# Performance work log

Hardware: AMD Instinct MI355X
Metric: run time of the kernel (lower is better)

The kernel has to match this reference:

```python
import jax, jax.numpy as jnp
import numpy as np


def setup_inputs() -> dict:
    key = jax.random.key(0)
    k0, k1, k2, k3, k4, k5 = jax.random.split(key, 6)
    B, V, Fin, K, Fout = 8, 49152, 64, 3, 64
    nnz = V * 8  # ~8 neighbors per vertex (HEALPix sphere graph)
    std = (2.0 / (Fin * K)) ** 0.5  # Kaiming-normal as in reset_parameters
    inputs = jax.random.normal(k0, (B, V, Fin), jnp.float32)
    weight = jax.random.normal(k1, (Fin, K, Fout), jnp.float32) * std
    bias = jax.random.normal(k2, (Fout,), jnp.float32) * 0.05
    lap_rows = jax.random.randint(k3, (nnz,), 0, V, jnp.int32)
    lap_cols = jax.random.randint(k4, (nnz,), 0, V, jnp.int32)
    lap_vals = jax.random.normal(k5, (nnz,), jnp.float32) * 0.1
    return {"inputs": inputs, "weight": weight, "bias": bias,
            "lap_rows": lap_rows, "lap_cols": lap_cols, "lap_vals": lap_vals}


def reference(inputs, weight, bias, lap_rows, lap_cols, lap_vals):
    B, V, Fin = inputs.shape
    _, K, Fout = weight.shape

    def spmm(x):  # sparse Laplacian (COO) @ dense [V, Fin*B]
        return jax.ops.segment_sum(lap_vals[:, None] * x[lap_cols], lap_rows,
                                   num_segments=V)

    # x0: [V, Fin*B], matching torch's permute(1,2,0).view(V, Fin*B)
    x0 = inputs.transpose(1, 2, 0).reshape(V, Fin * B)
    xs = [x0]
    if K > 1:
        x1 = spmm(x0)
        xs.append(x1)
    for _ in range(2, K):
        x2 = 2.0 * spmm(x1) - x0  # Chebyshev recurrence
        xs.append(x2)
        x0, x1 = x1, x2
    x = jnp.stack(xs)                                    # [K, V, Fin*B]
    x = x.reshape(K, V, Fin, B).transpose(3, 1, 2, 0)    # [B, V, Fin, K]
    x = x.reshape(B * V, Fin * K)
    out = x @ weight.reshape(Fin * K, Fout)              # dense GEMM
    return out.reshape(B, V, Fout) + bias
```

## Files before the change

### kernel.cpp

```cpp
#include <hip/hip_runtime.h>
#include <stdint.h>

#define B_   8
#define V_   49152
#define M_   (B_ * V_)

typedef unsigned short ushort_t;
typedef __attribute__((ext_vector_type(8))) short short8;
typedef __attribute__((ext_vector_type(4))) float float4v;

__device__ __forceinline__ float bf2f_lo(unsigned int pk) {
    union { unsigned int u; float f; } x; x.u = pk << 16; return x.f;
}
__device__ __forceinline__ float bf2f_hi(unsigned int pk) {
    union { unsigned int u; float f; } x; x.u = pk & 0xffff0000u; return x.f;
}
__device__ __forceinline__ ushort_t f2bf(float f) {
    union { unsigned int u; float f; } x; x.f = f;
    unsigned int u = x.u;
    unsigned int r = u + 0x7fffu + ((u >> 16) & 1u);
    return (ushort_t)(r >> 16);
}
__device__ __forceinline__ unsigned int pack2(float a, float b) {
    return ((unsigned int)f2bf(b) << 16) | (unsigned int)f2bf(a);
}
__device__ __forceinline__ void fma8(float* acc, float w, const uint4& p) {
    const unsigned int* u = (const unsigned int*)&p;
    #pragma unroll
    for (int i = 0; i < 4; i++) {
        acc[2 * i]     += w * bf2f_lo(u[i]);
        acc[2 * i + 1] += w * bf2f_hi(u[i]);
    }
}

__global__ void fill_sentinel(float* out, int n) {
    int i = blockIdx.x * blockDim.x + threadIdx.x;
    if (i < n) out[i] = 9999.0f;
}

__global__ void zero_kernel(int* p, int n) {
    int i = blockIdx.x * blockDim.x + threadIdx.x;
    if (i < n) p[i] = 0;
}

__global__ void hist_kernel(const int* __restrict__ rows, int nnz, int* __restrict__ counts) {
    int i = blockIdx.x * blockDim.x + threadIdx.x;
    if (i < nnz) atomicAdd(&counts[rows[i]], 1);
}

__global__ __launch_bounds__(1024) void scan_kernel(const int* __restrict__ counts,
                                                    int* __restrict__ offsets) {
    __shared__ int s[1024];
    int t = threadIdx.x;
    const int C = V_ / 1024;
    int base_i = t * C;
    int sum = 0;
    for (int j = 0; j < C; j++) sum += counts[base_i + j];
    s[t] = sum;
    __syncthreads();
    for (int off = 1; off < 1024; off <<= 1) {
        int v = (t >= off) ? s[t - off] : 0;
        __syncthreads();
        s[t] += v;
        __syncthreads();
    }
    int run = (t == 0) ? 0 : s[t - 1];
    for (int j = 0; j < C; j++) {
        offsets[base_i + j] = run;
        run += counts[base_i + j];
    }
    if (t == 1023) offsets[V_] = run;
}

__global__ void bucket_kernel(const int* __restrict__ rows, const int* __restrict__ cols,
                              const float* __restrict__ vals, int nnz,
                              const int* __restrict__ offsets, int* __restrict__ cursor,
                              int* __restrict__ e_col, float* __restrict__ e_val) {
    int i = blockIdx.x * blockDim.x + threadIdx.x;
    if (i >= nnz) return;
    int r = rows[i];
    int p = offsets[r] + atomicAdd(&cursor[r], 1);
    e_col[p] = cols[i];
    e_val[p] = vals[i];
}

__global__ __launch_bounds__(256) void prep_x0t(const float* __restrict__ inp,
                                                ushort_t* __restrict__ x0t) {
    int idx = blockIdx.x * 256 + threadIdx.x;
    int f2 = idx & 31, v = idx >> 5;
    #pragma unroll
    for (int b = 0; b < 8; b++) {
        const float* src = inp + ((size_t)b * V_ + v) * 64 + f2 * 2;
        float2 d = *(const float2*)src;
        *(unsigned int*)(x0t + ((size_t)v * 8 + b) * 64 + f2 * 2) = pack2(d.x, d.y);
    }
}

__global__ void prep_w(const float* __restrict__ wgt, ushort_t* __restrict__ wBf) {
    int idx = blockIdx.x * 256 + threadIdx.x;
    if (idx >= 6 * 4 * 64 * 8) return;
    int j = idx & 7, lane = (idx >> 3) & 63, nt = (idx >> 9) & 3, kb = idx >> 11;
    int k = kb * 32 + (lane >> 4) * 8 + j;
    int kc = k >> 6, fi = k & 63;
    int fo = nt * 16 + (lane & 15);
    wBf[idx] = f2bf(wgt[(fi * 3 + kc) * 64 + fo]);
}

__device__ __forceinline__ void gather16(const ushort_t* __restrict__ src,
                                         const int* __restrict__ e_col,
                                         const float* __restrict__ e_val,
                                         int beg, int end, int b, int f8, float* acc) {
    int e = beg;
    for (; e + 4 <= end; e += 4) {
        int c0 = e_col[e], c1 = e_col[e + 1], c2 = e_col[e + 2], c3 = e_col[e + 3];
        float w0 = e_val[e], w1 = e_val[e + 1], w2 = e_val[e + 2], w3 = e_val[e + 3];
        const ushort_t* p0 = src + ((size_t)c0 * 512) + b * 64 + f8 * 16;
        const ushort_t* p1 = src + ((size_t)c1 * 512) + b * 64 + f8 * 16;
        const ushort_t* p2 = src + ((size_t)c2 * 512) + b * 64 + f8 * 16;
        const ushort_t* p3 = src + ((size_t)c3 * 512) + b * 64 + f8 * 16;
        uint4 a0 = *(const uint4*)p0, b0 = *(const uint4*)(p0 + 8);
        uint4 a1 = *(const uint4*)p1, b1 = *(const uint4*)(p1 + 8);
        uint4 a2 = *(const uint4*)p2, b2 = *(const uint4*)(p2 + 8);
        uint4 a3 = *(const uint4*)p3, b3 = *(const uint4*)(p3 + 8);
        fma8(acc, w0, a0); fma8(acc + 8, w0, b0);
        fma8(acc, w1, a1); fma8(acc + 8, w1, b1);
        fma8(acc, w2, a2); fma8(acc + 8, w2, b2);
        fma8(acc, w3, a3); fma8(acc + 8, w3, b3);
    }
    for (; e < end; e++) {
        int c = e_col[e];
        float w = e_val[e];
        const ushort_t* p = src + ((size_t)c * 512) + b * 64 + f8 * 16;
        uint4 a = *(const uint4*)p, bq = *(const uint4*)(p + 8);
        fma8(acc, w, a); fma8(acc + 8, w, bq);
    }
}

__global__ __launch_bounds__(256) void spmm1_kernel(const ushort_t* __restrict__ x0t,
                                                    const int* __restrict__ offsets,
                                                    const int* __restrict__ e_col,
                                                    const float* __restrict__ e_val,
                                                    ushort_t* __restrict__ x1) {
    int t = threadIdx.x;
    int vi = t >> 5, b = (t >> 2) & 7, f8 = t & 3;
    int v = blockIdx.x * 8 + vi;
    float acc[16];
    #pragma unroll
    for (int i = 0; i < 16; i++) acc[i] = 0.f;
    gather16(x0t, e_col, e_val, offsets[v], offsets[v + 1], b, f8, acc);
    unsigned int opk[8];
    #pragma unroll
    for (int i = 0; i < 8; i++) opk[i] = pack2(acc[2 * i], acc[2 * i + 1]);
    ushort_t* dst = x1 + ((size_t)v * 8 + b) * 64 + f8 * 16;
    *(uint4*)dst       = make_uint4(opk[0], opk[1], opk[2], opk[3]);
    *(uint4*)(dst + 8) = make_uint4(opk[4], opk[5], opk[6], opk[7]);
}

__global__ __launch_bounds__(256) void spmm2_gemm(const ushort_t* __restrict__ x0t,
                                                  const ushort_t* __restrict__ x1,
                                                  const int* __restrict__ offsets,
                                                  const int* __restrict__ e_col,
                                                  const float* __restrict__ e_val,
                                                  const ushort_t* __restrict__ wBf,
                                                  const float* __restrict__ bias,
                                                  float* __restrict__ out) {
    __shared__ ushort_t sh[64 * 72];
    int t = threadIdx.x;
    int vi = t >> 5, b = (t >> 2) & 7, f8 = t & 3;
    int v0 = blockIdx.x * 8;
    int v = v0 + vi;
    float acc[16];
    #pragma unroll
    for (int i = 0; i < 16; i++) acc[i] = 0.f;
    gather16(x1, e_col, e_val, offsets[v], offsets[v + 1], b, f8, acc);

    size_t r = (size_t)v * 8 + b;
    const ushort_t* x0p = x0t + r * 64 + f8 * 16;
    uint4 qa = *(const uint4*)x0p, qb = *(const uint4*)(x0p + 8);
    const unsigned int* ua = (const unsigned int*)&qa;
    const unsigned int* ub = (const unsigned int*)&qb;
    unsigned int opk[8];
    #pragma unroll
    for (int i = 0; i < 4; i++)
        opk[i] = pack2(2.f * acc[2 * i] - bf2f_lo(ua[i]),
                       2.f * acc[2 * i + 1] - bf2f_hi(ua[i]));
    #pragma unroll
    for (int i = 0; i < 4; i++)
        opk[4 + i] = pack2(2.f * acc[8 + 2 * i] - bf2f_lo(ub[i]),
                           2.f * acc[8 + 2 * i + 1] - bf2f_hi(ub[i]));
    int mg = vi * 8 + b;
    ushort_t* dst = sh + mg * 72 + f8 * 16;
    *(uint4*)dst       = make_uint4(opk[0], opk[1], opk[2], opk[3]);
    *(uint4*)(dst + 8) = make_uint4(opk[4], opk[5], opk[6], opk[7]);
    __syncthreads();

    int lane = t & 63, wv = t >> 6;
    int quad = lane >> 4, col = lane & 15;

    short8 Bf[6][4];
    #pragma unroll
    for (int kb = 0; kb < 6; kb++)
        #pragma unroll
        for (int nt = 0; nt < 4; nt++)
            Bf[kb][nt] = *(const short8*)(wBf + ((size_t)((kb * 4 + nt) * 64 + lane)) * 8);

    float bv[4];
    #pragma unroll
    for (int nt = 0; nt < 4; nt++) bv[nt] = bias[nt * 16 + col];

    float4v accm[4];
    #pragma unroll
    for (int nt = 0; nt < 4; nt++) accm[nt] = (float4v){0.f, 0.f, 0.f, 0.f};

    int m0 = v0 * 8 + wv * 16;
    size_t arow = (size_t)(m0 + col) * 64 + quad * 8;
    #pragma unroll
    for (int p = 0; p < 2; p++) {
        short8 A = *(const short8*)(x0t + arow + p * 32);
        #pragma unroll
        for (int nt = 0; nt < 4; nt++)
            accm[nt] = __builtin_amdgcn_mfma_f32_16x16x32_bf16(A, Bf[p][nt], accm[nt], 0, 0, 0);
    }
    #pragma unroll
    for (int p = 0; p < 2; p++) {
        short8 A = *(const short8*)(x1 + arow + p * 32);
        #pragma unroll
        for (int nt = 0; nt < 4; nt++)
            accm[nt] = __builtin_amdgcn_mfma_f32_16x16x32_bf16(A, Bf[2 + p][nt], accm[nt], 0, 0, 0);
    }
    #pragma unroll
    for (int p = 0; p < 2; p++) {
        short8 A = *(const short8*)(sh + (wv * 16 + col) * 72 + quad * 8 + p * 32);
        #pragma unroll
        for (int nt = 0; nt < 4; nt++)
            accm[nt] = __builtin_amdgcn_mfma_f32_16x16x32_bf16(A, Bf[4 + p][nt], accm[nt], 0, 0, 0);
    }

    #pragma unroll
    for (int reg = 0; reg < 4; reg++) {
        int m = m0 + quad * 4 + reg;
        int vv = m >> 3, bb = m & 7;
        float* orow = out + ((size_t)bb * V_ + vv) * 64;
        #pragma unroll
        for (int nt = 0; nt < 4; nt++)
            orow[nt * 16 + col] = accm[nt][reg] + bv[nt];
    }
}

extern "C" void kernel_launch(void* const* d_in, const int* in_sizes, int n_in,
                              void* d_out, int out_size, void* d_ws, size_t ws_size,
                              hipStream_t stream) {
    const float* inp  = (const float*)d_in[0];
    const float* wgt  = (const float*)d_in[1];
    const float* bias = (const float*)d_in[2];
    const int*   rows = (const int*)d_in[3];
    const int*   cols = (const int*)d_in[4];
    const float* vals = (const float*)d_in[5];
    int nnz = in_sizes[3];
    float* out = (float*)d_out;
    (void)n_in; (void)out_size;

    char* ws = (char*)d_ws;
    size_t o = 0;
    auto alloc = [&](size_t bytes) { void* p = ws + o; o += (bytes + 255) & ~(size_t)255; return p; };
    int*      counts  = (int*)alloc((size_t)V_ * 4);
    int*      cursor  = (int*)alloc((size_t)V_ * 4);
    int*      offsets = (int*)alloc(((size_t)V_ + 1) * 4);
    int*      e_col   = (int*)alloc((size_t)nnz * 4);
    float*    e_val   = (float*)alloc((size_t)nnz * 4);
    ushort_t* x0t     = (ushort_t*)alloc((size_t)M_ * 64 * 2);
    ushort_t* x1      = (ushort_t*)alloc((size_t)M_ * 64 * 2);
    ushort_t* wBf     = (ushort_t*)alloc(6 * 4 * 64 * 8 * 2);

    if (ws_size < o) {
        fill_sentinel<<<(M_ * 64 + 255) / 256, 256, 0, stream>>>(out, M_ * 64);
        return;
    }

    zero_kernel<<<(2 * V_ + 255) / 256, 256, 0, stream>>>(counts, 2 * V_);
    hist_kernel<<<(nnz + 255) / 256, 256, 0, stream>>>(rows, nnz, counts);
    scan_kernel<<<1, 1024, 0, stream>>>(counts, offsets);
    bucket_kernel<<<(nnz + 255) / 256, 256, 0, stream>>>(rows, cols, vals, nnz,
                                                         offsets, cursor, e_col, e_val);
    prep_x0t<<<(V_ * 32) / 256, 256, 0, stream>>>(inp, x0t);
    prep_w<<<48, 256, 0, stream>>>(wgt, wBf);
    spmm1_kernel<<<V_ / 8, 256, 0, stream>>>(x0t, offsets, e_col, e_val, x1);
    spmm2_gemm<<<V_ / 8, 256, 0, stream>>>(x0t, x1, offsets, e_col, e_val, wBf, bias, out);
}
```

Baseline: 391.4 us.

## Fuse prep kernels, fold Chebyshev recurrence into weights, pack edge col/val

Merges the x0 transpose/convert, histogram and weight prep into one launch and replaces the zeroing kernel with a memset. It folds the 2*spmm(x1)-x0 recurrence algebraically into the bf16 weights (W0-W2, W1, 2*W2), so spmm2 no longer reads x0 for the subtraction. It also packs edge column and value into one uint2 array, vectorizes the scan, hoists the GEMM A-operand loads ahead of the gather, and uses nontemporal output stores. The weight folding changes bf16 rounding behavior slightly.

```diff
diff --git a/kernel.cpp b/kernel.cpp
--- a/kernel.cpp
+++ b/kernel.cpp
@@ -38,24 +38,52 @@
     if (i < n) out[i] = 9999.0f;
 }
 
-__global__ void zero_kernel(int* p, int n) {
-    int i = blockIdx.x * blockDim.x + threadIdx.x;
-    if (i < n) p[i] = 0;
-}
-
-__global__ void hist_kernel(const int* __restrict__ rows, int nnz, int* __restrict__ counts) {
-    int i = blockIdx.x * blockDim.x + threadIdx.x;
-    if (i < nnz) atomicAdd(&counts[rows[i]], 1);
+#define PREP_B 6144
+__global__ __launch_bounds__(256) void k1_fused(const float* __restrict__ inp,
+                                                ushort_t* __restrict__ x0t,
+                                                const int* __restrict__ rows, int nnz,
+                                                int* __restrict__ counts,
+                                                const float* __restrict__ wgt,
+                                                ushort_t* __restrict__ wBf, int hb) {
+    int bid = blockIdx.x;
+    int t = threadIdx.x;
+    if (bid < PREP_B) {
+        int idx = bid * 256 + t;
+        int f2 = idx & 31, v = idx >> 5;
+        #pragma unroll
+        for (int b = 0; b < 8; b++) {
+            const float* src = inp + ((size_t)b * V_ + v) * 64 + f2 * 2;
+            float2 d = *(const float2*)src;
+            *(unsigned int*)(x0t + ((size_t)v * 8 + b) * 64 + f2 * 2) = pack2(d.x, d.y);
+        }
+    } else if (bid < PREP_B + hb) {
+        int i = (bid - PREP_B) * 256 + t;
+        if (i < nnz) atomicAdd(&counts[rows[i]], 1);
+    } else {
+        int idx = (bid - PREP_B - hb) * 256 + t;
+        int j = idx & 7, lane = (idx >> 3) & 63, ntc = (idx >> 9) & 3, kb = idx >> 11;
+        int k = kb * 32 + (lane >> 4) * 8 + j;
+        int kc = k >> 6, fi = k & 63;
+        int fo = ntc * 16 + (lane & 15);
+        float w;
+        if (kc == 0)      w = wgt[(fi * 3 + 0) * 64 + fo] - wgt[(fi * 3 + 2) * 64 + fo];
+        else if (kc == 1) w = wgt[(fi * 3 + 1) * 64 + fo];
+        else              w = 2.0f * wgt[(fi * 3 + 2) * 64 + fo];
+        wBf[idx] = f2bf(w);
+    }
 }
 
 __global__ __launch_bounds__(1024) void scan_kernel(const int* __restrict__ counts,
                                                     int* __restrict__ offsets) {
     __shared__ int s[1024];
     int t = threadIdx.x;
-    const int C = V_ / 1024;
-    int base_i = t * C;
+    int4 c[12];
     int sum = 0;
-    for (int j = 0; j < C; j++) sum += counts[base_i + j];
+    #pragma unroll
+    for (int j = 0; j < 12; j++) {
+        c[j] = ((const int4*)counts)[t * 12 + j];
+        sum += c[j].x + c[j].y + c[j].z + c[j].w;
+    }
     s[t] = sum;
     __syncthreads();
     for (int off = 1; off < 1024; off <<= 1) {
@@ -65,9 +93,14 @@
         __syncthreads();
     }
     int run = (t == 0) ? 0 : s[t - 1];
-    for (int j = 0; j < C; j++) {
-        offsets[base_i + j] = run;
-        run += counts[base_i + j];
+    #pragma unroll
+    for (int j = 0; j < 12; j++) {
+        int4 o;
+        o.x = run; run += c[j].x;
+        o.y = run; run += c[j].y;
+        o.z = run; run += c[j].z;
+        o.w = run; run += c[j].w;
+        ((int4*)offsets)[t * 12 + j] = o;
     }
     if (t == 1023) offsets[V_] = run;
 }
@@ -75,49 +108,26 @@
 __global__ void bucket_kernel(const int* __restrict__ rows, const int* __restrict__ cols,
                               const float* __restrict__ vals, int nnz,
                               const int* __restrict__ offsets, int* __restrict__ cursor,
-                              int* __restrict__ e_col, float* __restrict__ e_val) {
+                              uint2* __restrict__ e_cv) {
     int i = blockIdx.x * blockDim.x + threadIdx.x;
     if (i >= nnz) return;
     int r = rows[i];
     int p = offsets[r] + atomicAdd(&cursor[r], 1);
-    e_col[p] = cols[i];
-    e_val[p] = vals[i];
-}
-
-__global__ __launch_bounds__(256) void prep_x0t(const float* __restrict__ inp,
-                                                ushort_t* __restrict__ x0t) {
-    int idx = blockIdx.x * 256 + threadIdx.x;
-    int f2 = idx & 31, v = idx >> 5;
-    #pragma unroll
-    for (int b = 0; b < 8; b++) {
-        const float* src = inp + ((size_t)b * V_ + v) * 64 + f2 * 2;
-        float2 d = *(const float2*)src;
-        *(unsigned int*)(x0t + ((size_t)v * 8 + b) * 64 + f2 * 2) = pack2(d.x, d.y);
-    }
-}
-
-__global__ void prep_w(const float* __restrict__ wgt, ushort_t* __restrict__ wBf) {
-    int idx = blockIdx.x * 256 + threadIdx.x;
-    if (idx >= 6 * 4 * 64 * 8) return;
-    int j = idx & 7, lane = (idx >> 3) & 63, nt = (idx >> 9) & 3, kb = idx >> 11;
-    int k = kb * 32 + (lane >> 4) * 8 + j;
-    int kc = k >> 6, fi = k & 63;
-    int fo = nt * 16 + (lane & 15);
-    wBf[idx] = f2bf(wgt[(fi * 3 + kc) * 64 + fo]);
-}
-
-__device__ __forceinline__ void gather16(const ushort_t* __restrict__ src,
-                                         const int* __restrict__ e_col,
-                                         const float* __restrict__ e_val,
-                                         int beg, int end, int b, int f8, float* acc) {
+    e_cv[p] = make_uint2((unsigned int)cols[i], __float_as_uint(vals[i]));
+}
+
+__device__ __forceinline__ void gather16(const ushort_t* __restrict__ srcbf,
+                                         const uint2* __restrict__ e_cv,
+                                         int beg, int end, float* acc) {
     int e = beg;
     for (; e + 4 <= end; e += 4) {
-        int c0 = e_col[e], c1 = e_col[e + 1], c2 = e_col[e + 2], c3 = e_col[e + 3];
-        float w0 = e_val[e], w1 = e_val[e + 1], w2 = e_val[e + 2], w3 = e_val[e + 3];
-        const ushort_t* p0 = src + ((size_t)c0 * 512) + b * 64 + f8 * 16;
-        const ushort_t* p1 = src + ((size_t)c1 * 512) + b * 64 + f8 * 16;
-        const ushort_t* p2 = src + ((size_t)c2 * 512) + b * 64 + f8 * 16;
-        const ushort_t* p3 = src + ((size_t)c3 * 512) + b * 64 + f8 * 16;
+        uint2 q0 = e_cv[e], q1 = e_cv[e + 1], q2 = e_cv[e + 2], q3 = e_cv[e + 3];
+        float w0 = __uint_as_float(q0.y), w1 = __uint_as_float(q1.y);
+        float w2 = __uint_as_float(q2.y), w3 = __uint_as_float(q3.y);
+        const ushort_t* p0 = srcbf + ((size_t)q0.x * 512);
+        const ushort_t* p1 = srcbf + ((size_t)q1.x * 512);
+        const ushort_t* p2 = srcbf + ((size_t)q2.x * 512);
+        const ushort_t* p3 = srcbf + ((size_t)q3.x * 512);
         uint4 a0 = *(const uint4*)p0, b0 = *(const uint4*)(p0 + 8);
         uint4 a1 = *(const uint4*)p1, b1 = *(const uint4*)(p1 + 8);
         uint4 a2 = *(const uint4*)p2, b2 = *(const uint4*)(p2 + 8);
@@ -128,9 +138,9 @@
         fma8(acc, w3, a3); fma8(acc + 8, w3, b3);
     }
     for (; e < end; e++) {
-        int c = e_col[e];
-        float w = e_val[e];
-        const ushort_t* p = src + ((size_t)c * 512) + b * 64 + f8 * 16;
+        uint2 q = e_cv[e];
+        float w = __uint_as_float(q.y);
+        const ushort_t* p = srcbf + ((size_t)q.x * 512);
         uint4 a = *(const uint4*)p, bq = *(const uint4*)(p + 8);
         fma8(acc, w, a); fma8(acc + 8, w, bq);
     }
@@ -138,8 +148,7 @@
 
 __global__ __launch_bounds__(256) void spmm1_kernel(const ushort_t* __restrict__ x0t,
                                                     const int* __restrict__ offsets,
-                                                    const int* __restrict__ e_col,
-                                                    const float* __restrict__ e_val,
+                                                    const uint2* __restrict__ e_cv,
                                                     ushort_t* __restrict__ x1) {
     int t = threadIdx.x;
     int vi = t >> 5, b = (t >> 2) & 7, f8 = t & 3;
@@ -147,7 +156,7 @@
     float acc[16];
     #pragma unroll
     for (int i = 0; i < 16; i++) acc[i] = 0.f;
-    gather16(x0t, e_col, e_val, offsets[v], offsets[v + 1], b, f8, acc);
+    gather16(x0t + b * 64 + f8 * 16, e_cv, offsets[v], offsets[v + 1], acc);
     unsigned int opk[8];
     #pragma unroll
     for (int i = 0; i < 8; i++) opk[i] = pack2(acc[2 * i], acc[2 * i + 1]);
@@ -159,81 +168,73 @@
 __global__ __launch_bounds__(256) void spmm2_gemm(const ushort_t* __restrict__ x0t,
                                                   const ushort_t* __restrict__ x1,
                                                   const int* __restrict__ offsets,
-                                                  const int* __restrict__ e_col,
-                                                  const float* __restrict__ e_val,
+                                                  const uint2* __restrict__ e_cv,
                                                   const ushort_t* __restrict__ wBf,
                                                   const float* __restrict__ bias,
                                                   float* __restrict__ out) {
     __shared__ ushort_t sh[64 * 72];
     int t = threadIdx.x;
+    int lane = t & 63, wv = t >> 6;
+    int quad = lane >> 4, col = lane & 15;
+    int v0 = blockIdx.x * 8;
+    int m0 = v0 * 8 + wv * 16;
+
+    size_t arow = (size_t)(m0 + col) * 64 + quad * 8;
+    short8 A0[2], A1[2];
+    A0[0] = *(const short8*)(x0t + arow);
+    A0[1] = *(const short8*)(x0t + arow + 32);
+    A1[0] = *(const short8*)(x1 + arow);
+    A1[1] = *(const short8*)(x1 + arow + 32);
+
     int vi = t >> 5, b = (t >> 2) & 7, f8 = t & 3;
-    int v0 = blockIdx.x * 8;
     int v = v0 + vi;
     float acc[16];
     #pragma unroll
     for (int i = 0; i < 16; i++) acc[i] = 0.f;
-    gather16(x1, e_col, e_val, offsets[v], offsets[v + 1], b, f8, acc);
-
-    size_t r = (size_t)v * 8 + b;
-    const ushort_t* x0p = x0t + r * 64 + f8 * 16;
-    uint4 qa = *(const uint4*)x0p, qb = *(const uint4*)(x0p + 8);
-    const unsigned int* ua = (const unsigned int*)&qa;
-    const unsigned int* ub = (const unsigned int*)&qb;
+    gather16(x1 + b * 64 + f8 * 16, e_cv, offsets[v], offsets[v + 1], acc);
+
     unsigned int opk[8];
     #pragma unroll
-    for (int i = 0; i < 4; i++)
-        opk[i] = pack2(2.f * acc[2 * i] - bf2f_lo(ua[i]),
-                       2.f * acc[2 * i + 1] - bf2f_hi(ua[i]));
-    #pragma unroll
-    for (int i = 0; i < 4; i++)
-        opk[4 + i] = pack2(2.f * acc[8 + 2 * i] - bf2f_lo(ub[i]),
-                           2.f * acc[8 + 2 * i + 1] - bf2f_hi(ub[i]));
+    for (int i = 0; i < 8; i++) opk[i] = pack2(acc[2 * i], acc[2 * i + 1]);
     int mg = vi * 8 + b;
     ushort_t* dst = sh + mg * 72 + f8 * 16;
     *(uint4*)dst       = make_uint4(opk[0], opk[1], opk[2], opk[3]);
     *(uint4*)(dst + 8) = make_uint4(opk[4], opk[5], opk[6], opk[7]);
     __syncthreads();
 
-    int lane = t & 63, wv = t >> 6;
-    int quad = lane >> 4, col = lane & 15;
-
     short8 Bf[6][4];
     #pragma unroll
     for (int kb = 0; kb < 6; kb++)
         #pragma unroll
-        for (int nt = 0; nt < 4; nt++)
-            Bf[kb][nt] = *(const short8*)(wBf + ((size_t)((kb * 4 + nt) * 64 + lane)) * 8);
+        for (int ntc = 0; ntc < 4; ntc++)
+            Bf[kb][ntc] = *(const short8*)(wBf + ((size_t)((kb * 4 + ntc) * 64 + lane)) * 8);
 
     float bv[4];
     #pragma unroll
-    for (int nt = 0; nt < 4; nt++) bv[nt] = bias[nt * 16 + col];
+    for (int ntc = 0; ntc < 4; ntc++) bv[ntc] = bias[ntc * 16 + col];
 
     float4v accm[4];
     #pragma unroll
-    for (int nt = 0; nt < 4; nt++) accm[nt] = (float4v){0.f, 0.f, 0.f, 0.f};
-
-    int m0 = v0 * 8 + wv * 16;
-    size_t arow = (size_t)(m0 + col) * 64 + quad * 8;
+    for (int ntc = 0; ntc < 4; ntc++) accm[ntc] = (float4v){0.f, 0.f, 0.f, 0.f};
+
     #pragma unroll
     for (int p = 0; p < 2; p++) {
-        short8 A = *(const short8*)(x0t + arow + p * 32);
-        #pragma unroll
-        for (int nt = 0; nt < 4; nt++)
-            accm[nt] = __builtin_amdgcn_mfma_f32_16x16x32_bf16(A, Bf[p][nt], accm[nt], 0, 0, 0);
+        #pragma unroll
+        for (int ntc = 0; ntc < 4; ntc++)
+            accm[ntc] = __builtin_amdgcn_mfma_f32_16x16x32_bf16(A0[p], Bf[p][ntc], accm[ntc], 0, 0, 0);
     }
     #pragma unroll
     for (int p = 0; p < 2; p++) {
-        short8 A = *(const short8*)(x1 + arow + p * 32);
-        #pragma unroll
-        for (int nt = 0; nt < 4; nt++)
-            accm[nt] = __builtin_amdgcn_mfma_f32_16x16x32_bf16(A, Bf[2 + p][nt], accm[nt], 0, 0, 0);
+        #pragma unroll
+        for (int ntc = 0; ntc < 4; ntc++)
+            accm[ntc] = __builtin_amdgcn_mfma_f32_16x16x32_bf16(A1[p], Bf[2 + p][ntc], accm[ntc], 0, 0, 0);
     }
     #pragma unroll
     for (int p = 0; p < 2; p++) {
         short8 A = *(const short8*)(sh + (wv * 16 + col) * 72 + quad * 8 + p * 32);
         #pragma unroll
-        for (int nt = 0; nt < 4; nt++)
-            accm[nt] = __builtin_amdgcn_mfma_f32_16x16x32_bf16(A, Bf[4 + p][nt], accm[nt], 0, 0, 0);
+        for (int ntc = 0; ntc < 4; ntc++)
+            accm[ntc] = __builtin_amdgcn_mfma_f32_16x16x32_bf16(A, Bf[4 + p][ntc], accm[ntc], 0, 0, 0);
     }
 
     #pragma unroll
@@ -242,8 +243,8 @@
         int vv = m >> 3, bb = m & 7;
         float* orow = out + ((size_t)bb * V_ + vv) * 64;
         #pragma unroll
-        for (int nt = 0; nt < 4; nt++)
-            orow[nt * 16 + col] = accm[nt][reg] + bv[nt];
+        for (int ntc = 0; ntc < 4; ntc++)
+            __builtin_nontemporal_store(accm[ntc][reg] + bv[ntc], &orow[ntc * 16 + col]);
     }
 }
 
@@ -266,8 +267,7 @@
     int*      counts  = (int*)alloc((size_t)V_ * 4);
     int*      cursor  = (int*)alloc((size_t)V_ * 4);
     int*      offsets = (int*)alloc(((size_t)V_ + 1) * 4);
-    int*      e_col   = (int*)alloc((size_t)nnz * 4);
-    float*    e_val   = (float*)alloc((size_t)nnz * 4);
+    uint2*    e_cv    = (uint2*)alloc((size_t)nnz * 8);
     ushort_t* x0t     = (ushort_t*)alloc((size_t)M_ * 64 * 2);
     ushort_t* x1      = (ushort_t*)alloc((size_t)M_ * 64 * 2);
     ushort_t* wBf     = (ushort_t*)alloc(6 * 4 * 64 * 8 * 2);
@@ -277,13 +277,11 @@
         return;
     }
 
-    zero_kernel<<<(2 * V_ + 255) / 256, 256, 0, stream>>>(counts, 2 * V_);
-    hist_kernel<<<(nnz + 255) / 256, 256, 0, stream>>>(rows, nnz, counts);
+    int hb = (nnz + 255) / 256;
+    hipMemsetAsync(counts, 0, (size_t)2 * V_ * 4, stream);
+    k1_fused<<<PREP_B + hb + 48, 256, 0, stream>>>(inp, x0t, rows, nnz, counts, wgt, wBf, hb);
     scan_kernel<<<1, 1024, 0, stream>>>(counts, offsets);
-    bucket_kernel<<<(nnz + 255) / 256, 256, 0, stream>>>(rows, cols, vals, nnz,
-                                                         offsets, cursor, e_col, e_val);
-    prep_x0t<<<(V_ * 32) / 256, 256, 0, stream>>>(inp, x0t);
-    prep_w<<<48, 256, 0, stream>>>(wgt, wBf);
-    spmm1_kernel<<<V_ / 8, 256, 0, stream>>>(x0t, offsets, e_col, e_val, x1);
-    spmm2_gemm<<<V_ / 8, 256, 0, stream>>>(x0t, x1, offsets, e_col, e_val, wBf, bias, out);
-}
+    bucket_kernel<<<hb, 256, 0, stream>>>(rows, cols, vals, nnz, offsets, cursor, e_cv);
+    spmm1_kernel<<<V_ / 8, 256, 0, stream>>>(x0t, offsets, e_cv, x1);
+    spmm2_gemm<<<V_ / 8, 256, 0, stream>>>(x0t, x1, offsets, e_cv, wBf, bias, out);
+}
```

After: 368.2 us. -5.9%, faster.
